# Optimization experiments

Measured on AMD Instinct MI355X. Metric: run time of the kernel, lower is better.

## Reference

```python
import jax, jax.numpy as jnp
from jax import lax
import numpy as np

PAD_IDX = 4
KERNEL_SIZES = (2, 3, 4, 5)
N_FILTERS = 32
D_EMB = 8
D_OUT = 64
VOCAB = 5
B, L = 4096, 512
LN_EPS = 1e-5


def setup_inputs() -> dict:
    key = jax.random.key(0)
    ks = jax.random.split(key, 32)
    inp = {}
    inp['x_idx'] = jax.random.randint(ks[0], (B, L), 0, VOCAB, dtype=jnp.int64 if jax.config.jax_enable_x64 else jnp.int32)
    emb = jax.random.normal(ks[1], (VOCAB, D_EMB), dtype=jnp.float32) * 0.1
    inp['emb'] = emb.at[PAD_IDX].set(0.0)  # padding_idx row zero
    for i, kz in enumerate(KERNEL_SIZES):
        inp[f'conv_w{i}'] = jax.random.normal(ks[2 + 2 * i], (N_FILTERS, D_EMB, kz), dtype=jnp.float32) * (1.0 / np.sqrt(D_EMB * kz))
        inp[f'conv_b{i}'] = jnp.zeros((N_FILTERS,), jnp.float32)
        inp[f'att_w{i}'] = jax.random.normal(ks[3 + 2 * i], (N_FILTERS,), dtype=jnp.float32) * (1.0 / np.sqrt(N_FILTERS))
        inp[f'att_b{i}'] = jnp.zeros((1,), jnp.float32)
    inp['proj_w'] = jax.random.normal(ks[20], (D_OUT, N_FILTERS * len(KERNEL_SIZES)), dtype=jnp.float32) * (1.0 / np.sqrt(N_FILTERS * len(KERNEL_SIZES)))
    inp['proj_b'] = jnp.zeros((D_OUT,), jnp.float32)
    inp['gamma'] = jnp.ones((D_OUT,), jnp.float32)
    inp['beta'] = jnp.zeros((D_OUT,), jnp.float32)
    return inp


def _branch(X, W, b, aw, ab):
    # X: [B, C_in, L]; W: [C_out, C_in, ks]
    h = lax.conv_general_dilated(X, W, (1,), 'VALID',
                                 dimension_numbers=('NCH', 'OIH', 'NCH'))
    h = jax.nn.gelu(h + b[None, :, None], approximate=False)     # [B, F, L']
    scores = jnp.einsum('bfl,f->bl', h, aw) + ab[0]              # linear attn score
    w = jax.nn.softmax(scores, axis=1)                           # over positions
    return jnp.einsum('bfl,bl->bf', h, w)                        # weighted pool -> [B, F]


def reference(x_idx, emb, conv_w0, conv_b0, conv_w1, conv_b1, conv_w2, conv_b2,
              conv_w3, conv_b3, att_w0, att_b0, att_w1, att_b1, att_w2, att_b2,
              att_w3, att_b3, proj_w, proj_b, gamma, beta):
    emb = emb.at[PAD_IDX].set(0.0)
    X = emb[x_idx].transpose(0, 2, 1)  # [B, d_emb, L]
    feats = [
        _branch(X, conv_w0, conv_b0, att_w0, att_b0),
        _branch(X, conv_w1, conv_b1, att_w1, att_b1),
        _branch(X, conv_w2, conv_b2, att_w2, att_b2),
        _branch(X, conv_w3, conv_b3, att_w3, att_b3),
    ]
    z = jnp.concatenate(feats, axis=1)                 # [B, 4*F]
    z = z @ proj_w.T + proj_b                          # [B, D_OUT]
    z = jax.nn.gelu(z, approximate=False)
    mu = jnp.mean(z, axis=-1, keepdims=True)
    var = jnp.var(z, axis=-1, keepdims=True)
    return (z - mu) / jnp.sqrt(var + LN_EPS) * gamma + beta
```

## Files before the change

### kernel.cpp

```cpp
#include <hip/hip_runtime.h>
#include <math.h>

typedef _Float16 half_t;
typedef _Float16 half8 __attribute__((ext_vector_type(8)));

#define BATCH 4096
#define SEQL  512
#define NF    32
#define DEMB  8
#define DOUT  64

#define NWIN_TOTAL 3900
#define HWIN_OFF   4096
#define TOFF       70000

__device__ __forceinline__ float gelu_exact(float x) {
    return 0.5f * x * (1.0f + erff(x * 0.70710678118654752f));
}

__global__ __launch_bounds__(256) void precompute_taps(
    const float* __restrict__ emb,
    const float* __restrict__ cw0, const float* __restrict__ cw1,
    const float* __restrict__ cw2, const float* __restrict__ cw3,
    float* __restrict__ ws)
{
    const int gid = blockIdx.x * blockDim.x + threadIdx.x;
    if (gid >= 14 * 5 * NF) return;
    const int f = gid & 31;
    const int r = gid >> 5;
    const int tapg = r / 5;
    const int d    = r % 5;

    int ks, t; const float* cw;
    if (tapg < 2)      { ks = 2; cw = cw0; t = tapg; }
    else if (tapg < 5) { ks = 3; cw = cw1; t = tapg - 2; }
    else if (tapg < 9) { ks = 4; cw = cw2; t = tapg - 5; }
    else               { ks = 5; cw = cw3; t = tapg - 9; }

    const float* e = emb + d * DEMB;
    float s = 0.0f;
#pragma unroll
    for (int c = 0; c < DEMB; ++c)
        s += e[c] * cw[(f * DEMB + c) * ks + t];
    ws[TOFF + r * NF + f] = s;
}

__global__ __launch_bounds__(256) void precompute_windows(
    const float* __restrict__ cb0, const float* __restrict__ aw0, const float* __restrict__ ab0,
    const float* __restrict__ cb1, const float* __restrict__ aw1, const float* __restrict__ ab1,
    const float* __restrict__ cb2, const float* __restrict__ aw2, const float* __restrict__ ab2,
    const float* __restrict__ cb3, const float* __restrict__ aw3, const float* __restrict__ ab3,
    float* __restrict__ ws)
{
    const int gid = blockIdx.x * blockDim.x + threadIdx.x;
    if (gid >= NWIN_TOTAL * NF) return;
    const int wgid = gid >> 5;
    const int f    = gid & 31;

    int w, ks, cum;
    const float *cb, *aw, *ab;
    if (wgid < 25)       { w = wgid;       ks = 2; cum = 0; cb = cb0; aw = aw0; ab = ab0; }
    else if (wgid < 150) { w = wgid - 25;  ks = 3; cum = 2; cb = cb1; aw = aw1; ab = ab1; }
    else if (wgid < 775) { w = wgid - 150; ks = 4; cum = 5; cb = cb2; aw = aw2; ab = ab2; }
    else                 { w = wgid - 775; ks = 5; cum = 9; cb = cb3; aw = aw3; ab = ab3; }

    float h = cb[f];
    int ww = w;
    for (int t = ks - 1; t >= 0; --t) {
        int d = ww % 5; ww /= 5;
        h += ws[TOFF + ((cum + t) * 5 + d) * NF + f];
    }
    float g = gelu_exact(h);
    ((half_t*)(ws + HWIN_OFF))[wgid * NF + f] = (half_t)g;

    float s = g * aw[f];
#pragma unroll
    for (int off = 16; off; off >>= 1) s += __shfl_xor(s, off, 32);
    if (f == 0) ws[wgid] = s + ab[0];
}

__global__ __launch_bounds__(256) void fused_main(
    const int*   __restrict__ xidx,
    const float* __restrict__ ws,
    const float* __restrict__ projw, const float* __restrict__ projb,
    const float* __restrict__ gamma, const float* __restrict__ beta,
    float* __restrict__ out)
{
    __shared__ int   xs[SEQL];
    __shared__ float pwS[4][SEQL];
    __shared__ int   poffS[4][SEQL];
    __shared__ float feat[4 * NF];

    const int b   = blockIdx.x;
    const int tid = threadIdx.x;
    const half_t* hwin16 = (const half_t*)(ws + HWIN_OFF);

#pragma unroll
    for (int i = tid; i < SEQL / 4; i += 256)
        ((int4*)xs)[i] = ((const int4*)(xidx + b * SEQL))[i];
    __syncthreads();

    const int wave = tid >> 6;
    const int lane = tid & 63;

    constexpr int KS[4]  = {2, 3, 4, 5};
    constexpr int SWB[4] = {0, 25, 150, 775};

    const int ks = KS[wave];
    const int Lp = SEQL + 1 - ks;
    const float* swin = ws + SWB[wave];
    const half_t* tab = hwin16 + SWB[wave] * NF;

    {
        float sv[8];
        float m = -INFINITY;
#pragma unroll
        for (int it = 0; it < 8; ++it) {
            int l = lane + it * 64;
            int w = 0; float s = -INFINITY;
            if (l < Lp) {
                w = xs[l];
                for (int t = 1; t < ks; ++t) w = w * 5 + xs[l + t];
                s = swin[w];
            }
            poffS[wave][l] = w << 6;
            sv[it] = s;
            m = fmaxf(m, s);
        }
#pragma unroll
        for (int off = 32; off; off >>= 1) m = fmaxf(m, __shfl_xor(m, off));

        float ssum = 0.0f;
#pragma unroll
        for (int it = 0; it < 8; ++it) {
            sv[it] = __expf(sv[it] - m);
            ssum += sv[it];
        }
#pragma unroll
        for (int off = 32; off; off >>= 1) ssum += __shfl_xor(ssum, off);
        const float inv = 1.0f / ssum;
#pragma unroll
        for (int it = 0; it < 8; ++it)
            pwS[wave][lane + it * 64] = sv[it] * inv;
    }
    __syncthreads();

    const int quad = lane & 3;
    const int pg   = lane >> 2;

    float a[8];
#pragma unroll
    for (int j = 0; j < 8; ++j) a[j] = 0.0f;

#pragma unroll 8
    for (int it = 0; it < 32; ++it) {
        const int pos = it * 16 + pg;
        const float p = pwS[wave][pos];
        const int  off = poffS[wave][pos];
        half8 r = *(const half8*)((const char*)tab + off + quad * 16);
#pragma unroll
        for (int j = 0; j < 8; ++j)
            a[j] += p * (float)r[j];
    }

#pragma unroll
    for (int off = 4; off < 64; off <<= 1) {
#pragma unroll
        for (int j = 0; j < 8; ++j) a[j] += __shfl_xor(a[j], off);
    }
    if (lane < 4) {
        float* fp = feat + wave * NF + lane * 8;
#pragma unroll
        for (int j = 0; j < 8; ++j) fp[j] = a[j];
    }
    __syncthreads();

    if (tid < DOUT) {
        float z = projb[tid];
        const float4* pwr = (const float4*)(projw + tid * (4 * NF));
#pragma unroll
        for (int q = 0; q < 32; ++q) {
            float4 wq = pwr[q];
            const float* fj = feat + q * 4;
            z += wq.x * fj[0] + wq.y * fj[1] + wq.z * fj[2] + wq.w * fj[3];
        }
        z = gelu_exact(z);

        float s1 = z, s2 = z * z;
#pragma unroll
        for (int off = 32; off; off >>= 1) {
            s1 += __shfl_xor(s1, off);
            s2 += __shfl_xor(s2, off);
        }
        const float mu  = s1 * (1.0f / 64.0f);
        const float var = s2 * (1.0f / 64.0f) - mu * mu;
        const float r   = rsqrtf(var + 1e-5f);
        out[b * DOUT + tid] = (z - mu) * r * gamma[tid] + beta[tid];
    }
}

extern "C" void kernel_launch(void* const* d_in, const int* in_sizes, int n_in,
                              void* d_out, int out_size, void* d_ws, size_t ws_size,
                              hipStream_t stream) {
    const int*   xidx = (const int*)d_in[0];
    const float* emb  = (const float*)d_in[1];
    const float* cw[4]; const float* cb[4]; const float* aw[4]; const float* ab[4];
    for (int i = 0; i < 4; ++i) {
        cw[i] = (const float*)d_in[2 + 4 * i];
        cb[i] = (const float*)d_in[3 + 4 * i];
        aw[i] = (const float*)d_in[4 + 4 * i];
        ab[i] = (const float*)d_in[5 + 4 * i];
    }
    const float* projw = (const float*)d_in[18];
    const float* projb = (const float*)d_in[19];
    const float* gm    = (const float*)d_in[20];
    const float* bt    = (const float*)d_in[21];
    float* ws  = (float*)d_ws;
    float* out = (float*)d_out;

    hipLaunchKernelGGL(precompute_taps, dim3((14 * 5 * NF + 255) / 256), dim3(256), 0, stream,
                       emb, cw[0], cw[1], cw[2], cw[3], ws);

    hipLaunchKernelGGL(precompute_windows, dim3((NWIN_TOTAL * NF + 255) / 256), dim3(256), 0, stream,
                       cb[0], aw[0], ab[0],
                       cb[1], aw[1], ab[1],
                       cb[2], aw[2], ab[2],
                       cb[3], aw[3], ab[3],
                       ws);

    hipLaunchKernelGGL(fused_main, dim3(BATCH), dim3(256), 0, stream,
                       xidx, ws, projw, projb, gm, bt, out);
}
```

Baseline: 148.8 us.

## Split pooled gather by position range across waves for all branches

Each wave now gathers a quarter of the positions for every one of the four branches, instead of one wave handling all positions of a single branch. The branches have tables of very different sizes (25 to 3125 windows), so this spreads the cache-heavy gathers from the large tables across all waves and balances the load. Window indices are stored as 16-bit values in shared memory rather than precomputed byte offsets, which reduces LDS footprint. The cost is more accumulator registers (32 floats), four times the shuffle reductions, an extra shared partial-sum buffer, and an extra barrier plus a cross-wave sum step.

New measurement: 194.9 us. +31.0%, slower.

```diff
diff --git a/kernel.cpp b/kernel.cpp
--- a/kernel.cpp
+++ b/kernel.cpp
@@ -3,6 +3,7 @@
 
 typedef _Float16 half_t;
 typedef _Float16 half8 __attribute__((ext_vector_type(8)));
+typedef unsigned short ushort_t;
 
 #define BATCH 4096
 #define SEQL  512
@@ -86,10 +87,11 @@
     const float* __restrict__ gamma, const float* __restrict__ beta,
     float* __restrict__ out)
 {
-    __shared__ int   xs[SEQL];
-    __shared__ float pwS[4][SEQL];
-    __shared__ int   poffS[4][SEQL];
-    __shared__ float feat[4 * NF];
+    __shared__ int      xs[SEQL];
+    __shared__ float    pwS[4][SEQL];
+    __shared__ ushort_t pwid[4][SEQL];
+    __shared__ float    partial[4][4][NF];
+    __shared__ float    feat[4 * NF];
 
     const int b   = blockIdx.x;
     const int tid = threadIdx.x;
@@ -106,12 +108,11 @@
     constexpr int KS[4]  = {2, 3, 4, 5};
     constexpr int SWB[4] = {0, 25, 150, 775};
 
-    const int ks = KS[wave];
-    const int Lp = SEQL + 1 - ks;
-    const float* swin = ws + SWB[wave];
-    const half_t* tab = hwin16 + SWB[wave] * NF;
-
     {
+        const int ks = KS[wave];
+        const int Lp = SEQL + 1 - ks;
+        const float* swin = ws + SWB[wave];
+
         float sv[8];
         float m = -INFINITY;
 #pragma unroll
@@ -123,7 +124,7 @@
                 for (int t = 1; t < ks; ++t) w = w * 5 + xs[l + t];
                 s = swin[w];
             }
-            poffS[wave][l] = w << 6;
+            pwid[wave][l] = (ushort_t)w;
             sv[it] = s;
             m = fmaxf(m, s);
         }
@@ -148,30 +149,49 @@
     const int quad = lane & 3;
     const int pg   = lane >> 2;
 
-    float a[8];
-#pragma unroll
-    for (int j = 0; j < 8; ++j) a[j] = 0.0f;
-
-#pragma unroll 8
-    for (int it = 0; it < 32; ++it) {
-        const int pos = it * 16 + pg;
-        const float p = pwS[wave][pos];
-        const int  off = poffS[wave][pos];
-        half8 r = *(const half8*)((const char*)tab + off + quad * 16);
-#pragma unroll
-        for (int j = 0; j < 8; ++j)
-            a[j] += p * (float)r[j];
-    }
-
-#pragma unroll
-    for (int off = 4; off < 64; off <<= 1) {
-#pragma unroll
-        for (int j = 0; j < 8; ++j) a[j] += __shfl_xor(a[j], off);
-    }
-    if (lane < 4) {
-        float* fp = feat + wave * NF + lane * 8;
-#pragma unroll
-        for (int j = 0; j < 8; ++j) fp[j] = a[j];
+    float acc[4][8];
+#pragma unroll
+    for (int k = 0; k < 4; ++k)
+#pragma unroll
+        for (int j = 0; j < 8; ++j) acc[k][j] = 0.0f;
+
+#pragma unroll
+    for (int k = 0; k < 4; ++k) {
+        const int c = (wave + k) & 3;
+        const int swb_b = (c == 0) ? 0 : (c == 1) ? 25 * NF * 2
+                        : (c == 2) ? 150 * NF * 2 : 775 * NF * 2;
+        const char* tabc = (const char*)hwin16 + swb_b;
+#pragma unroll
+        for (int it = 0; it < 8; ++it) {
+            const int pos = (wave << 7) + (it << 4) + pg;
+            const float p = pwS[c][pos];
+            const int  off = ((int)pwid[c][pos]) << 6;
+            half8 r = *(const half8*)(tabc + off + quad * 16);
+#pragma unroll
+            for (int j = 0; j < 8; ++j)
+                acc[k][j] += p * (float)r[j];
+        }
+    }
+
+#pragma unroll
+    for (int k = 0; k < 4; ++k) {
+        const int c = (wave + k) & 3;
+#pragma unroll
+        for (int j = 0; j < 8; ++j) {
+            float v = acc[k][j];
+            v += __shfl_xor(v, 4);
+            v += __shfl_xor(v, 8);
+            v += __shfl_xor(v, 16);
+            v += __shfl_xor(v, 32);
+            if (lane < 4) partial[wave][c][lane * 8 + j] = v;
+        }
+    }
+    __syncthreads();
+
+    if (tid < 128) {
+        const int c = tid >> 5, f = tid & 31;
+        feat[c * NF + f] = partial[0][c][f] + partial[1][c][f]
+                         + partial[2][c][f] + partial[3][c][f];
     }
     __syncthreads();
 
```

## Split each conv branch across two waves with 512-thread blocks

Applied to the files above, without the earlier changes.

The main kernel now launches 512 threads per batch row, and each conv branch is handled by two waves that each cover half of the sequence. The softmax max and sum are combined across the two waves through shared memory, and the pooled partial features are summed before the projection. Window ids are stored as 16-bit values instead of precomputed int offsets, which cuts shared memory use. The goal is more parallelism and shorter per-wave serial loops, in exchange for extra barriers and reduction steps.

Result: no change. 151.5 us (+1.8%).

```diff
diff --git a/kernel.cpp b/kernel.cpp
--- a/kernel.cpp
+++ b/kernel.cpp
@@ -3,6 +3,7 @@
 
 typedef _Float16 half_t;
 typedef _Float16 half8 __attribute__((ext_vector_type(8)));
+typedef unsigned short ushort_t;
 
 #define BATCH 4096
 #define SEQL  512
@@ -79,84 +80,93 @@
     if (f == 0) ws[wgid] = s + ab[0];
 }
 
-__global__ __launch_bounds__(256) void fused_main(
+__global__ __launch_bounds__(512, 8) void fused_main(
     const int*   __restrict__ xidx,
     const float* __restrict__ ws,
     const float* __restrict__ projw, const float* __restrict__ projb,
     const float* __restrict__ gamma, const float* __restrict__ beta,
     float* __restrict__ out)
 {
-    __shared__ int   xs[SEQL];
-    __shared__ float pwS[4][SEQL];
-    __shared__ int   poffS[4][SEQL];
-    __shared__ float feat[4 * NF];
+    __shared__ int      xs[SEQL];
+    __shared__ float    pwS[4][SEQL];
+    __shared__ ushort_t pwid[4][SEQL];
+    __shared__ float    partial[8][NF];
+    __shared__ float    red_m[8], red_s[8];
+    __shared__ float    feat[4 * NF];
 
     const int b   = blockIdx.x;
     const int tid = threadIdx.x;
     const half_t* hwin16 = (const half_t*)(ws + HWIN_OFF);
 
 #pragma unroll
-    for (int i = tid; i < SEQL / 4; i += 256)
+    for (int i = tid; i < SEQL / 4; i += 512)
         ((int4*)xs)[i] = ((const int4*)(xidx + b * SEQL))[i];
     __syncthreads();
 
     const int wave = tid >> 6;
     const int lane = tid & 63;
+    const int c    = wave & 3;
+    const int hh   = wave >> 2;
 
     constexpr int KS[4]  = {2, 3, 4, 5};
     constexpr int SWB[4] = {0, 25, 150, 775};
 
-    const int ks = KS[wave];
+    const int ks = KS[c];
     const int Lp = SEQL + 1 - ks;
-    const float* swin = ws + SWB[wave];
-    const half_t* tab = hwin16 + SWB[wave] * NF;
-
+    const float* swin = ws + SWB[c];
+
+    float sv[4];
     {
-        float sv[8];
         float m = -INFINITY;
 #pragma unroll
-        for (int it = 0; it < 8; ++it) {
-            int l = lane + it * 64;
+        for (int it = 0; it < 4; ++it) {
+            int l = hh * 256 + it * 64 + lane;
             int w = 0; float s = -INFINITY;
             if (l < Lp) {
                 w = xs[l];
                 for (int t = 1; t < ks; ++t) w = w * 5 + xs[l + t];
                 s = swin[w];
             }
-            poffS[wave][l] = w << 6;
+            pwid[c][l] = (ushort_t)w;
             sv[it] = s;
             m = fmaxf(m, s);
         }
 #pragma unroll
         for (int off = 32; off; off >>= 1) m = fmaxf(m, __shfl_xor(m, off));
+        if (lane == 0) red_m[wave] = m;
+        __syncthreads();
+        m = fmaxf(red_m[c], red_m[c + 4]);
 
         float ssum = 0.0f;
 #pragma unroll
-        for (int it = 0; it < 8; ++it) {
+        for (int it = 0; it < 4; ++it) {
             sv[it] = __expf(sv[it] - m);
             ssum += sv[it];
         }
 #pragma unroll
         for (int off = 32; off; off >>= 1) ssum += __shfl_xor(ssum, off);
-        const float inv = 1.0f / ssum;
-#pragma unroll
-        for (int it = 0; it < 8; ++it)
-            pwS[wave][lane + it * 64] = sv[it] * inv;
+        if (lane == 0) red_s[wave] = ssum;
+        __syncthreads();
+        const float inv = 1.0f / (red_s[c] + red_s[c + 4]);
+#pragma unroll
+        for (int it = 0; it < 4; ++it)
+            pwS[c][hh * 256 + it * 64 + lane] = sv[it] * inv;
     }
     __syncthreads();
 
     const int quad = lane & 3;
     const int pg   = lane >> 2;
+    const half_t* tab = hwin16 + SWB[c] * NF;
 
     float a[8];
 #pragma unroll
     for (int j = 0; j < 8; ++j) a[j] = 0.0f;
 
 #pragma unroll 8
-    for (int it = 0; it < 32; ++it) {
-        const int pos = it * 16 + pg;
-        const float p = pwS[wave][pos];
-        const int  off = poffS[wave][pos];
+    for (int it = 0; it < 16; ++it) {
+        const int pos = hh * 256 + it * 16 + pg;
+        const float p = pwS[c][pos];
+        const int  off = ((int)pwid[c][pos]) << 6;
         half8 r = *(const half8*)((const char*)tab + off + quad * 16);
 #pragma unroll
         for (int j = 0; j < 8; ++j)
@@ -169,9 +179,15 @@
         for (int j = 0; j < 8; ++j) a[j] += __shfl_xor(a[j], off);
     }
     if (lane < 4) {
-        float* fp = feat + wave * NF + lane * 8;
+        float* fp = partial[wave] + lane * 8;
 #pragma unroll
         for (int j = 0; j < 8; ++j) fp[j] = a[j];
+    }
+    __syncthreads();
+
+    if (tid < 128) {
+        const int c2 = tid >> 5, f = tid & 31;
+        feat[c2 * NF + f] = partial[c2][f] + partial[c2 + 4][f];
     }
     __syncthreads();
 
@@ -228,6 +244,6 @@
                        cb[3], aw[3], ab[3],
                        ws);
 
-    hipLaunchKernelGGL(fused_main, dim3(BATCH), dim3(256), 0, stream,
+    hipLaunchKernelGGL(fused_main, dim3(BATCH), dim3(512), 0, stream,
                        xidx, ws, projw, projb, gm, bt, out);
 }
```

## Fold softmax numerators into precomputed exp-weighted window table with shared denominator

Applied to the files above, without the earlier changes.

Adds a kernel that precomputes, per window id, the fp16 row exp(score - 8) * gelu_h and the scalar exp(score - 8) in a padded 128-byte row. The main kernel then skips the per-position softmax (max reduction, exp, normalise, shared-memory weights). It sums the pre-weighted rows plus the denominator and divides once at the end. Shared memory drops to 16-bit window ids. This relies on a fixed shift constant instead of the true max, so overflow, underflow or fp16 precision loss can occur if scores stray far from the shift.

Result: slower. 163.2 us (+9.7%).

```diff
diff --git a/kernel.cpp b/kernel.cpp
--- a/kernel.cpp
+++ b/kernel.cpp
@@ -3,6 +3,7 @@
 
 typedef _Float16 half_t;
 typedef _Float16 half8 __attribute__((ext_vector_type(8)));
+typedef unsigned short ushort_t;
 
 #define BATCH 4096
 #define SEQL  512
@@ -11,8 +12,11 @@
 #define DOUT  64
 
 #define NWIN_TOTAL 3900
+#define ZROW       3900
 #define HWIN_OFF   4096
 #define TOFF       70000
+#define EHE_OFF    131072
+#define MSHIFT     8.0f
 
 __device__ __forceinline__ float gelu_exact(float x) {
     return 0.5f * x * (1.0f + erff(x * 0.70710678118654752f));
@@ -79,6 +83,29 @@
     if (f == 0) ws[wgid] = s + ab[0];
 }
 
+__global__ __launch_bounds__(256) void finalize_ehe(float* __restrict__ ws)
+{
+    const int gid = blockIdx.x * blockDim.x + threadIdx.x;
+    if (gid >= (NWIN_TOTAL + 1) * 8) return;
+    const int row = gid >> 3;
+    const int seg = gid & 7;
+
+    float4 v = {0.f, 0.f, 0.f, 0.f};
+    if (row < NWIN_TOTAL) {
+        const float E = __expf(ws[row] - MSHIFT);
+        if (seg < 4) {
+            const half_t* h = (const half_t*)(ws + HWIN_OFF) + row * NF + seg * 8;
+            half_t o[8];
+#pragma unroll
+            for (int j = 0; j < 8; ++j) o[j] = (half_t)(E * (float)h[j]);
+            v = *(const float4*)o;
+        } else if (seg == 4) {
+            v.x = E;
+        }
+    }
+    *(float4*)((char*)(ws + EHE_OFF) + row * 128 + seg * 16) = v;
+}
+
 __global__ __launch_bounds__(256) void fused_main(
     const int*   __restrict__ xidx,
     const float* __restrict__ ws,
@@ -86,14 +113,12 @@
     const float* __restrict__ gamma, const float* __restrict__ beta,
     float* __restrict__ out)
 {
-    __shared__ int   xs[SEQL];
-    __shared__ float pwS[4][SEQL];
-    __shared__ int   poffS[4][SEQL];
-    __shared__ float feat[4 * NF];
+    __shared__ int      xs[SEQL];
+    __shared__ ushort_t pwid[4][SEQL];
+    __shared__ float    feat[4 * NF];
 
     const int b   = blockIdx.x;
     const int tid = threadIdx.x;
-    const half_t* hwin16 = (const half_t*)(ws + HWIN_OFF);
 
 #pragma unroll
     for (int i = tid; i < SEQL / 4; i += 256)
@@ -108,70 +133,56 @@
 
     const int ks = KS[wave];
     const int Lp = SEQL + 1 - ks;
-    const float* swin = ws + SWB[wave];
-    const half_t* tab = hwin16 + SWB[wave] * NF;
-
-    {
-        float sv[8];
-        float m = -INFINITY;
-#pragma unroll
-        for (int it = 0; it < 8; ++it) {
-            int l = lane + it * 64;
-            int w = 0; float s = -INFINITY;
-            if (l < Lp) {
-                w = xs[l];
-                for (int t = 1; t < ks; ++t) w = w * 5 + xs[l + t];
-                s = swin[w];
-            }
-            poffS[wave][l] = w << 6;
-            sv[it] = s;
-            m = fmaxf(m, s);
-        }
-#pragma unroll
-        for (int off = 32; off; off >>= 1) m = fmaxf(m, __shfl_xor(m, off));
-
-        float ssum = 0.0f;
-#pragma unroll
-        for (int it = 0; it < 8; ++it) {
-            sv[it] = __expf(sv[it] - m);
-            ssum += sv[it];
-        }
-#pragma unroll
-        for (int off = 32; off; off >>= 1) ssum += __shfl_xor(ssum, off);
-        const float inv = 1.0f / ssum;
-#pragma unroll
-        for (int it = 0; it < 8; ++it)
-            pwS[wave][lane + it * 64] = sv[it] * inv;
+
+#pragma unroll
+    for (int it = 0; it < 8; ++it) {
+        const int l = lane + it * 64;
+        ushort_t v = ZROW;
+        if (l < Lp) {
+            int w = xs[l];
+            for (int t = 1; t < ks; ++t) w = w * 5 + xs[l + t];
+            v = (ushort_t)(SWB[wave] + w);
+        }
+        pwid[wave][l] = v;
     }
     __syncthreads();
 
-    const int quad = lane & 3;
-    const int pg   = lane >> 2;
+    const int r = lane & 7;
+    const int o = lane >> 3;
+    const int seg = (r < 4) ? r : 4;
+    const char* base = (const char*)(ws + EHE_OFF) + seg * 16;
 
     float a[8];
 #pragma unroll
     for (int j = 0; j < 8; ++j) a[j] = 0.0f;
+    float den = 0.0f;
 
 #pragma unroll 8
-    for (int it = 0; it < 32; ++it) {
-        const int pos = it * 16 + pg;
-        const float p = pwS[wave][pos];
-        const int  off = poffS[wave][pos];
-        half8 r = *(const half8*)((const char*)tab + off + quad * 16);
-#pragma unroll
-        for (int j = 0; j < 8; ++j)
-            a[j] += p * (float)r[j];
-    }
-
-#pragma unroll
-    for (int off = 4; off < 64; off <<= 1) {
+    for (int it = 0; it < 64; ++it) {
+        const int pos = it * 8 + o;
+        const int gid = pwid[wave][pos];
+        const float4 rv = *(const float4*)(base + gid * 128);
+        if (r < 4) {
+            const half8 hv = *(const half8*)&rv;
+#pragma unroll
+            for (int j = 0; j < 8; ++j) a[j] += (float)hv[j];
+        } else if (r == 4) {
+            den += rv.x;
+        }
+    }
+
+#pragma unroll
+    for (int off = 8; off < 64; off <<= 1) {
 #pragma unroll
         for (int j = 0; j < 8; ++j) a[j] += __shfl_xor(a[j], off);
-    }
+        den += __shfl_xor(den, off);
+    }
+    const float dtot = __shfl(den, 4);
     if (lane < 4) {
+        const float inv = 1.0f / dtot;
         float* fp = feat + wave * NF + lane * 8;
 #pragma unroll
-        for (int j = 0; j < 8; ++j) fp[j] = a[j];
+        for (int j = 0; j < 8; ++j) fp[j] = a[j] * inv;
     }
     __syncthreads();
 
@@ -194,8 +205,8 @@
         }
         const float mu  = s1 * (1.0f / 64.0f);
         const float var = s2 * (1.0f / 64.0f) - mu * mu;
-        const float r   = rsqrtf(var + 1e-5f);
-        out[b * DOUT + tid] = (z - mu) * r * gamma[tid] + beta[tid];
+        const float rr  = rsqrtf(var + 1e-5f);
+        out[b * DOUT + tid] = (z - mu) * rr * gamma[tid] + beta[tid];
     }
 }
 
@@ -228,6 +239,9 @@
                        cb[3], aw[3], ab[3],
                        ws);
 
+    hipLaunchKernelGGL(finalize_ehe, dim3(((NWIN_TOTAL + 1) * 8 + 255) / 256), dim3(256), 0, stream,
+                       ws);
+
     hipLaunchKernelGGL(fused_main, dim3(BATCH), dim3(256), 0, stream,
                        xidx, ws, projw, projb, gm, bt, out);
 }
```
